# Kernel tuning notes

Measured on AMD Instinct MI355X. Metric: run time of the kernel, lower is better.

Reference implementation:

```python
import jax, jax.numpy as jnp
import numpy as np

B, TK, H = 32, 8192, 256

def setup_inputs() -> dict:
    key = jax.random.key(0)
    ks = jax.random.split(key, 10)
    s = 0.02
    return {
        "s_t_hat": jax.random.normal(ks[0], (B, 2 * H), dtype=jnp.float32),
        "encoder_outputs": jax.random.normal(ks[1], (B, TK, H), dtype=jnp.float32),
        "enc_padding_mask": jnp.ones((B, TK), dtype=jnp.float32),
        "coverage": jax.random.uniform(ks[2], (B, TK), dtype=jnp.float32),
        "attn_dist_node_to_token": jax.random.uniform(ks[3], (B, TK), dtype=jnp.float32),
        "We": jax.random.normal(ks[4], (H, H), dtype=jnp.float32) * s,   # encode_proj weight
        "Wd": jax.random.normal(ks[5], (H, 2 * H), dtype=jnp.float32) * s,  # decode_proj weight
        "bd": jax.random.normal(ks[6], (H,), dtype=jnp.float32) * s,     # decode_proj bias
        "wc": jax.random.normal(ks[7], (H,), dtype=jnp.float32) * s,     # W_c weight (Linear(1,H))
        "v": jax.random.normal(ks[8], (H,), dtype=jnp.float32) * s,      # v weight (Linear(H,1))
    }

def reference(s_t_hat, encoder_outputs, enc_padding_mask, coverage,
              attn_dist_node_to_token, We, Wd, bd, wc, v):
    # encoder projection: [b,t,h] @ We^T -> [b,t,h]
    enc_feat = jnp.einsum('bth,gh->btg', encoder_outputs, We)
    # decoder projection: [b,2h] @ Wd^T + bd -> [b,h]
    dec_fea = s_t_hat @ Wd.T + bd
    # coverage feature: outer product coverage[b,t] x wc[h]
    att_features = enc_feat + dec_fea[:, None, :] + coverage[..., None] * wc
    e = jnp.tanh(att_features)
    scores = jnp.einsum('bth,h->bt', e, v)  # [b, t_k]
    attn_ = jax.nn.softmax(scores, axis=1) * enc_padding_mask
    attn = attn_ / jnp.sum(attn_, axis=1, keepdims=True)
    c_t = jnp.einsum('bt,bth->bh', attn, encoder_outputs)  # context
    new_cov = jnp.clip(coverage + attn, 0.0, 1.0)
    return (c_t, attn, new_cov)
```

## Files before the change

### kernel.cpp

```cpp
#include <hip/hip_runtime.h>

#define B_  32
#define TK_ 8192
#define H_  256
#define SR  32
#define NS  8
#define NBX 32

typedef __bf16 bf16_t;
typedef __bf16 bf16x4 __attribute__((ext_vector_type(4)));
typedef __bf16 bf16x8 __attribute__((ext_vector_type(8)));
typedef float  floatx4 __attribute__((ext_vector_type(4)));

__device__ __forceinline__ float tanh_fast(float x) {
    float e = __builtin_amdgcn_exp2f(x * 2.885390081777927f);
    return 1.0f - 2.0f * __builtin_amdgcn_rcpf(e + 1.0f);
}

__global__ void prep_kernel(const float* __restrict__ s_t_hat,
                            const float* __restrict__ We,
                            const float* __restrict__ Wd,
                            const float* __restrict__ bd,
                            bf16_t* __restrict__ We_bf,
                            float* __restrict__ dec_ws) {
    int tid = threadIdx.x, blk = blockIdx.x;
    int gid = blk * 256 + tid;
    We_bf[gid] = (bf16_t)We[gid];

    if (blk >= 32 && blk < 160) {
        int idx  = (blk - 32) * 256 + tid;
        int pair = idx >> 2, q = idx & 3;
        int b = pair >> 8, i = pair & 255;
        const float4* sp = (const float4*)(s_t_hat + b * 2 * H_ + q * 128);
        const float4* wp = (const float4*)(Wd + (size_t)i * 2 * H_ + q * 128);
        float sum = 0.f;
        #pragma unroll 8
        for (int ii = 0; ii < 32; ++ii) {
            float4 a = sp[ii], w = wp[ii];
            sum += a.x * w.x + a.y * w.y + a.z * w.z + a.w * w.w;
        }
        sum += __shfl_xor(sum, 1, 64);
        sum += __shfl_xor(sum, 2, 64);
        if (q == 0) dec_ws[pair] = sum + bd[i];
    }
}

__global__ __launch_bounds__(256, 4) void attn_main(
    const float* __restrict__ enc,
    const float* __restrict__ mask,
    const float* __restrict__ cov,
    const float* __restrict__ wc,
    const float* __restrict__ v,
    const bf16_t* __restrict__ We_bf,
    const float* __restrict__ dec_ws,
    float* __restrict__ ctx_part,
    float* __restrict__ D_part,
    float* __restrict__ attn_out) {

    __shared__ __align__(16) bf16_t As[2][SR * 264];
    __shared__ float sp[4][SR];
    __shared__ float ctxp[4][256];
    __shared__ float cov_s[256], mask_s[256];

    const int tid  = threadIdx.x;
    const int b    = blockIdx.y;
    const int xb   = blockIdx.x;
    const int lane = tid & 63, w = tid >> 6;
    const int l15  = lane & 15, l4 = lane >> 4;
    const int t0b  = xb * (NS * SR);

    const int wbase = w * 64;
    float decv[4], wcv[4], vv[4];
    #pragma unroll
    for (int ni = 0; ni < 4; ++ni) {
        int g = wbase + ni * 16 + l15;
        decv[ni] = dec_ws[b * H_ + g];
        wcv[ni]  = wc[g];
        vv[ni]   = v[g];
    }

    const float* encb = enc + ((size_t)b * TK_ + t0b) * H_;
    const int colh = lane * 4;

    cov_s[tid]  = cov[(size_t)b * TK_ + t0b + tid];
    mask_s[tid] = mask[(size_t)b * TK_ + t0b + tid];
    #pragma unroll
    for (int it = 0; it < 8; ++it) {
        int row = it * 4 + w;
        float4 f = *(const float4*)(encb + (size_t)row * H_ + colh);
        bf16x4 q; q[0]=(bf16_t)f.x; q[1]=(bf16_t)f.y; q[2]=(bf16_t)f.z; q[3]=(bf16_t)f.w;
        *(bf16x4*)(&As[0][row * 264 + colh]) = q;
    }
    __syncthreads();

    float c0=0.f, c1=0.f, c2=0.f, c3=0.f;
    float d_tot = 0.f;
    int p = 0;

    for (int s = 0; s < NS; ++s) {
        const int tl0 = s * SR;

        floatx4 acc[2][4];
        #pragma unroll
        for (int mi = 0; mi < 2; ++mi)
            #pragma unroll
            for (int ni = 0; ni < 4; ++ni)
                acc[mi][ni] = (floatx4){0.f, 0.f, 0.f, 0.f};

        #pragma unroll
        for (int ks = 0; ks < 8; ++ks) {
            const int k = ks * 32 + l4 * 8;
            bf16x8 a0 = *(const bf16x8*)(&As[p][(     l15) * 264 + k]);
            bf16x8 a1 = *(const bf16x8*)(&As[p][(16 + l15) * 264 + k]);
            bf16x8 bq[4];
            #pragma unroll
            for (int ni = 0; ni < 4; ++ni)
                bq[ni] = *(const bf16x8*)(We_bf + (size_t)(wbase + ni * 16 + l15) * H_ + k);
            #pragma unroll
            for (int ni = 0; ni < 4; ++ni) {
                acc[0][ni] = __builtin_amdgcn_mfma_f32_16x16x32_bf16(a0, bq[ni], acc[0][ni], 0, 0, 0);
                acc[1][ni] = __builtin_amdgcn_mfma_f32_16x16x32_bf16(a1, bq[ni], acc[1][ni], 0, 0, 0);
            }
        }

        if (s < NS - 1) {
            const float* nb = encb + (size_t)(s + 1) * SR * H_;
            #pragma unroll
            for (int it = 0; it < 8; ++it) {
                int row = it * 4 + w;
                float4 f = *(const float4*)(nb + (size_t)row * H_ + colh);
                bf16x4 q; q[0]=(bf16_t)f.x; q[1]=(bf16_t)f.y; q[2]=(bf16_t)f.z; q[3]=(bf16_t)f.w;
                *(bf16x4*)(&As[p ^ 1][row * 264 + colh]) = q;
            }
        }

        #pragma unroll
        for (int mi = 0; mi < 2; ++mi) {
            #pragma unroll
            for (int r = 0; r < 4; ++r) {
                int tl = mi * 16 + l4 * 4 + r;
                float cv = cov_s[tl0 + tl];
                float ssum = 0.f;
                #pragma unroll
                for (int ni = 0; ni < 4; ++ni) {
                    float af = acc[mi][ni][r] + decv[ni] + cv * wcv[ni];
                    ssum += tanh_fast(af) * vv[ni];
                }
                ssum += __shfl_xor(ssum, 1, 64);
                ssum += __shfl_xor(ssum, 2, 64);
                ssum += __shfl_xor(ssum, 4, 64);
                ssum += __shfl_xor(ssum, 8, 64);
                if (l15 == 0) sp[w][tl] = ssum;
            }
        }
        __syncthreads();

        #pragma unroll
        for (int j = 0; j < 8; ++j) {
            int t = w * 8 + j;
            float sc = sp[0][t] + sp[1][t] + sp[2][t] + sp[3][t];
            float wv = __builtin_amdgcn_exp2f(sc * 1.4426950408889634f)
                       * mask_s[tl0 + t];
            if (lane == 0) {
                attn_out[(size_t)b * TK_ + t0b + tl0 + t] = wv;
                d_tot += wv;
            }
            bf16x4 q = *(const bf16x4*)(&As[p][t * 264 + colh]);
            c0 += wv * (float)q[0];
            c1 += wv * (float)q[1];
            c2 += wv * (float)q[2];
            c3 += wv * (float)q[3];
        }
        __syncthreads();
        p ^= 1;
    }

    if (lane == 0) sp[w][0] = d_tot;
    *(float4*)(&ctxp[w][colh]) = (float4){c0, c1, c2, c3};
    __syncthreads();
    float sctx = ctxp[0][tid] + ctxp[1][tid] + ctxp[2][tid] + ctxp[3][tid];
    ctx_part[((size_t)b * NBX + xb) * H_ + tid] = sctx;
    if (tid == 0) D_part[b * NBX + xb] = sp[0][0] + sp[1][0] + sp[2][0] + sp[3][0];
}

__global__ void finalize_kernel(const float* __restrict__ cov,
                                const float* __restrict__ ctx_part,
                                const float* __restrict__ D_part,
                                float* __restrict__ out) {
    int b = blockIdx.y, chunk = blockIdx.x, tid = threadIdx.x;
    int lane = tid & 63;

    float dv = (lane < NBX) ? D_part[b * NBX + lane] : 0.f;
    dv += __shfl_xor(dv, 1, 64);  dv += __shfl_xor(dv, 2, 64);
    dv += __shfl_xor(dv, 4, 64);  dv += __shfl_xor(dv, 8, 64);
    dv += __shfl_xor(dv, 16, 64); dv += __shfl_xor(dv, 32, 64);
    float invD = 1.0f / dv;

    int idx = chunk * 256 + tid;
    size_t gi = (size_t)b * TK_ + idx;
    float* attn = out + 8192;
    float* ncov = out + 8192 + (size_t)B_ * TK_;
    float a = attn[gi] * invD;
    attn[gi] = a;
    float nc = cov[gi] + a;
    ncov[gi] = fminf(fmaxf(nc, 0.f), 1.f);

    if (chunk == 0) {
        const float* cp = ctx_part + (size_t)b * NBX * H_ + tid;
        float s = 0.f;
        #pragma unroll
        for (int x = 0; x < NBX; ++x) s += cp[(size_t)x * H_];
        out[b * 256 + tid] = s * invD;
    }
}

extern "C" void kernel_launch(void* const* d_in, const int* in_sizes, int n_in,
                              void* d_out, int out_size, void* d_ws, size_t ws_size,
                              hipStream_t stream) {
    const float* s_t_hat = (const float*)d_in[0];
    const float* enc     = (const float*)d_in[1];
    const float* mask    = (const float*)d_in[2];
    const float* cov     = (const float*)d_in[3];
    const float* We      = (const float*)d_in[5];
    const float* Wd      = (const float*)d_in[6];
    const float* bd      = (const float*)d_in[7];
    const float* wc      = (const float*)d_in[8];
    const float* v       = (const float*)d_in[9];
    float* out = (float*)d_out;

    char* ws = (char*)d_ws;
    bf16_t* We_bf    = (bf16_t*)ws;
    float*  dec_ws   = (float*)(ws + 131072);
    float*  D_part   = (float*)(ws + 131072 + 32768);
    float*  ctx_part = (float*)(ws + 131072 + 32768 + 4096);

    prep_kernel<<<256, 256, 0, stream>>>(s_t_hat, We, Wd, bd, We_bf, dec_ws);
    attn_main<<<dim3(NBX, 32), 256, 0, stream>>>(enc, mask, cov, wc, v, We_bf,
                                                 dec_ws, ctx_part, D_part, out + 8192);
    finalize_kernel<<<dim3(32, 32), 256, 0, stream>>>(cov, ctx_part, D_part, out);
}
```

Baseline: 505.8 us.

## Stream encoder tiles into swizzled fp32 LDS via async loads and keep We in registers

The encoder tile for the next stage is now loaded straight from global memory into LDS with global_load_lds. It is issued before the current stage's MFMA work, instead of being loaded into registers, converted to bf16 and stored afterwards. The LDS tile stays fp32 with an XOR swizzle, and conversion to bf16 happens when operands are read for the MFMA. The bf16 We fragments are now loaded once per wave into registers rather than re-read from global memory on every k-step. Each block now covers twice as many timesteps with half as many blocks and a lower occupancy hint, which raises register and LDS use per block.

```diff
diff --git a/kernel.cpp b/kernel.cpp
--- a/kernel.cpp
+++ b/kernel.cpp
@@ -4,11 +4,10 @@
 #define TK_ 8192
 #define H_  256
 #define SR  32
-#define NS  8
-#define NBX 32
+#define NS  16
+#define NBX 16
 
 typedef __bf16 bf16_t;
-typedef __bf16 bf16x4 __attribute__((ext_vector_type(4)));
 typedef __bf16 bf16x8 __attribute__((ext_vector_type(8)));
 typedef float  floatx4 __attribute__((ext_vector_type(4)));
 
@@ -45,7 +44,7 @@
     }
 }
 
-__global__ __launch_bounds__(256, 4) void attn_main(
+__global__ __launch_bounds__(256, 2) void attn_main(
     const float* __restrict__ enc,
     const float* __restrict__ mask,
     const float* __restrict__ cov,
@@ -57,10 +56,10 @@
     float* __restrict__ D_part,
     float* __restrict__ attn_out) {
 
-    __shared__ __align__(16) bf16_t As[2][SR * 264];
+    __shared__ __align__(16) float As32[2][SR * 256];
     __shared__ float sp[4][SR];
     __shared__ float ctxp[4][256];
-    __shared__ float cov_s[256], mask_s[256];
+    __shared__ float cov_s[NS * SR], mask_s[NS * SR];
 
     const int tid  = threadIdx.x;
     const int b    = blockIdx.y;
@@ -78,28 +77,49 @@
         wcv[ni]  = wc[g];
         vv[ni]   = v[g];
     }
+    bf16x8 bq[4][8];
+    #pragma unroll
+    for (int ni = 0; ni < 4; ++ni)
+        #pragma unroll
+        for (int ks = 0; ks < 8; ++ks)
+            bq[ni][ks] = *(const bf16x8*)(We_bf + (size_t)(wbase + ni * 16 + l15) * H_
+                                          + ks * 32 + l4 * 8);
 
     const float* encb = enc + ((size_t)b * TK_ + t0b) * H_;
-    const int colh = lane * 4;
-
-    cov_s[tid]  = cov[(size_t)b * TK_ + t0b + tid];
-    mask_s[tid] = mask[(size_t)b * TK_ + t0b + tid];
-    #pragma unroll
-    for (int it = 0; it < 8; ++it) {
-        int row = it * 4 + w;
-        float4 f = *(const float4*)(encb + (size_t)row * H_ + colh);
-        bf16x4 q; q[0]=(bf16_t)f.x; q[1]=(bf16_t)f.y; q[2]=(bf16_t)f.z; q[3]=(bf16_t)f.w;
-        *(bf16x4*)(&As[0][row * 264 + colh]) = q;
-    }
+
+    cov_s[tid]        = cov[(size_t)b * TK_ + t0b + tid];
+    cov_s[tid + 256]  = cov[(size_t)b * TK_ + t0b + tid + 256];
+    mask_s[tid]       = mask[(size_t)b * TK_ + t0b + tid];
+    mask_s[tid + 256] = mask[(size_t)b * TK_ + t0b + tid + 256];
+
+    #define STAGE(buf, sidx)                                                     \
+    {                                                                            \
+        const float* nb_ = encb + (size_t)(sidx) * SR * H_;                      \
+        _Pragma("unroll")                                                        \
+        for (int it_ = 0; it_ < 8; ++it_) {                                      \
+            int row_ = it_ * 4 + w;                                              \
+            const float* g_ = nb_ + (size_t)row_ * H_                            \
+                              + ((lane * 4) ^ ((row_ & 7) << 2));                \
+            __builtin_amdgcn_global_load_lds(                                    \
+                (const __attribute__((address_space(1))) void*)g_,               \
+                (__attribute__((address_space(3))) void*)&As32[buf][row_ * 256], \
+                16, 0, 0);                                                       \
+        }                                                                        \
+    }
+
+    STAGE(0, 0)
     __syncthreads();
 
-    float c0=0.f, c1=0.f, c2=0.f, c3=0.f;
+    float c0 = 0.f, c1 = 0.f, c2 = 0.f, c3 = 0.f;
     float d_tot = 0.f;
     int p = 0;
 
     for (int s = 0; s < NS; ++s) {
         const int tl0 = s * SR;
 
+        if (s < NS - 1) STAGE(p ^ 1, s + 1)
+
+        const float* Ap = &As32[p][0];
         floatx4 acc[2][4];
         #pragma unroll
         for (int mi = 0; mi < 2; ++mi)
@@ -109,28 +129,25 @@
 
         #pragma unroll
         for (int ks = 0; ks < 8; ++ks) {
-            const int k = ks * 32 + l4 * 8;
-            bf16x8 a0 = *(const bf16x8*)(&As[p][(     l15) * 264 + k]);
-            bf16x8 a1 = *(const bf16x8*)(&As[p][(16 + l15) * 264 + k]);
-            bf16x8 bq[4];
-            #pragma unroll
-            for (int ni = 0; ni < 4; ++ni)
-                bq[ni] = *(const bf16x8*)(We_bf + (size_t)(wbase + ni * 16 + l15) * H_ + k);
+            const int rb = ks * 128 + l4 * 32;
+            bf16x8 av[2];
+            #pragma unroll
+            for (int mi = 0; mi < 2; ++mi) {
+                int row = mi * 16 + l15;
+                int sw  = (row & 7) << 4;
+                floatx4 f0 = *(const floatx4*)((const char*)(Ap + row * 256) + ((rb     ) ^ sw));
+                floatx4 f1 = *(const floatx4*)((const char*)(Ap + row * 256) + ((rb + 16) ^ sw));
+                bf16x8 a_;
+                a_[0] = (bf16_t)f0.x; a_[1] = (bf16_t)f0.y;
+                a_[2] = (bf16_t)f0.z; a_[3] = (bf16_t)f0.w;
+                a_[4] = (bf16_t)f1.x; a_[5] = (bf16_t)f1.y;
+                a_[6] = (bf16_t)f1.z; a_[7] = (bf16_t)f1.w;
+                av[mi] = a_;
+            }
             #pragma unroll
             for (int ni = 0; ni < 4; ++ni) {
-                acc[0][ni] = __builtin_amdgcn_mfma_f32_16x16x32_bf16(a0, bq[ni], acc[0][ni], 0, 0, 0);
-                acc[1][ni] = __builtin_amdgcn_mfma_f32_16x16x32_bf16(a1, bq[ni], acc[1][ni], 0, 0, 0);
-            }
-        }
-
-        if (s < NS - 1) {
-            const float* nb = encb + (size_t)(s + 1) * SR * H_;
-            #pragma unroll
-            for (int it = 0; it < 8; ++it) {
-                int row = it * 4 + w;
-                float4 f = *(const float4*)(nb + (size_t)row * H_ + colh);
-                bf16x4 q; q[0]=(bf16_t)f.x; q[1]=(bf16_t)f.y; q[2]=(bf16_t)f.z; q[3]=(bf16_t)f.w;
-                *(bf16x4*)(&As[p ^ 1][row * 264 + colh]) = q;
+                acc[0][ni] = __builtin_amdgcn_mfma_f32_16x16x32_bf16(av[0], bq[ni][ks], acc[0][ni], 0, 0, 0);
+                acc[1][ni] = __builtin_amdgcn_mfma_f32_16x16x32_bf16(av[1], bq[ni][ks], acc[1][ni], 0, 0, 0);
             }
         }
 
@@ -165,18 +182,23 @@
                 attn_out[(size_t)b * TK_ + t0b + tl0 + t] = wv;
                 d_tot += wv;
             }
-            bf16x4 q = *(const bf16x4*)(&As[p][t * 264 + colh]);
-            c0 += wv * (float)q[0];
-            c1 += wv * (float)q[1];
-            c2 += wv * (float)q[2];
-            c3 += wv * (float)q[3];
+            floatx4 q = *(const floatx4*)((const char*)(Ap + t * 256)
+                                          + ((lane * 16) ^ ((t & 7) << 4)));
+            c0 += wv * q.x;
+            c1 += wv * q.y;
+            c2 += wv * q.z;
+            c3 += wv * q.w;
         }
         __syncthreads();
         p ^= 1;
     }
 
     if (lane == 0) sp[w][0] = d_tot;
-    *(float4*)(&ctxp[w][colh]) = (float4){c0, c1, c2, c3};
+    {
+        int h0 = lane * 4;
+        ctxp[w][h0 + 0] = c0; ctxp[w][h0 + 1] = c1;
+        ctxp[w][h0 + 2] = c2; ctxp[w][h0 + 3] = c3;
+    }
     __syncthreads();
     float sctx = ctxp[0][tid] + ctxp[1][tid] + ctxp[2][tid] + ctxp[3][tid];
     ctx_part[((size_t)b * NBX + xb) * H_ + tid] = sctx;
@@ -232,7 +254,7 @@
     bf16_t* We_bf    = (bf16_t*)ws;
     float*  dec_ws   = (float*)(ws + 131072);
     float*  D_part   = (float*)(ws + 131072 + 32768);
-    float*  ctx_part = (float*)(ws + 131072 + 32768 + 4096);
+    float*  ctx_part = (float*)(ws + 131072 + 32768 + 2048);
 
     prep_kernel<<<256, 256, 0, stream>>>(s_t_hat, We, Wd, bd, We_bf, dec_ws);
     attn_main<<<dim3(NBX, 32), 256, 0, stream>>>(enc, mask, cov, wc, v, We_bf,
```

After: 406.9 us. 1.24x faster.
